# Optimization experiments

Hardware: AMD Instinct MI355X
Metric: run time of the kernel (lower is better)

## Reference

```python
import jax, jax.numpy as jnp
import numpy as np
from jax import lax

# Model config (matches init_kwargs)
SEL = [128, 128]          # radial neighbors per type
A_SEL = [16, 16]          # angular neighbors per type
LAYERS = [256, 256, 256]  # hidden layer sizes, final output dim is 1
N_ATOMS = 4096
N_TYPES = 2
D_DESC = sum(SEL) + 3 * sum(A_SEL)  # 352
BOX = 40.0
EPS = 1e-16


def setup_inputs() -> dict:
    key = jax.random.key(0)
    ks = jax.random.split(key, 16)
    xyz = jax.random.uniform(ks[0], (N_ATOMS, 3), jnp.float32) * BOX
    box_size = jnp.full((3,), BOX, jnp.float32)
    atomtypes = jax.random.randint(ks[1], (N_ATOMS,), 0, N_TYPES, jnp.int32)
    dims = [D_DESC] + LAYERS + [1]
    params = {}
    ki = 2
    for l in range(len(dims) - 1):
        params[f'w{l+1}'] = (jax.random.normal(ks[ki], (N_TYPES, dims[l], dims[l+1]), jnp.float32)
                             / np.sqrt(dims[l]).astype(np.float32))
        params[f'b{l+1}'] = jnp.zeros((N_TYPES, dims[l+1]), jnp.float32)
        ki += 1
    return {'xyz': xyz, 'box_size': box_size, 'atomtypes': atomtypes, **params}


def _descriptors(xyz, box_size, atomtypes):
    """PBC distance matrix + per-type top-k neighbors + DeePMD local-frame descriptor."""
    N = xyz.shape[0]
    # minimum-image displacement (N, N, 3) and distance (N, N)
    dm = xyz[:, None, :] - xyz[None, :, :] + EPS
    dm = dm - box_size * jnp.round(dm / box_size)
    dist = jnp.sqrt(jnp.sum(dm * dm, axis=-1))
    diag = jnp.eye(N, dtype=bool)

    blocks, a_xyz_l, a_dist_l = [], [], []
    lf_dist = lf_idx = None
    for j, selj in enumerate(SEL):
        mask = (atomtypes == j)[None, :] & (~diag)
        dists = jnp.where(mask, dist, jnp.inf)
        # full torch.sort only ever uses the first max(selj, a_selj, 2) columns -> top_k
        k = max(selj, A_SEL[j], 2)
        neg_top, idx = lax.top_k(-dists, k)
        sd = -neg_top  # sorted ascending distances, (N, k)
        if j == 0:
            lf_dist, lf_idx = sd[:, :2], idx[:, :2]
        else:
            cd = jnp.concatenate([lf_dist, sd[:, :2]], axis=1)
            ci = jnp.concatenate([lf_idx, idx[:, :2]], axis=1)
            order = jnp.argsort(cd, axis=1)
            lf_dist = jnp.take_along_axis(cd, order, axis=1)[:, :2]
            lf_idx = jnp.take_along_axis(ci, order, axis=1)[:, :2]
        blocks.append(1.0 / (sd[:, :selj] + EPS))  # inverse-distance radial block
        a_xyz_l.append(jnp.take_along_axis(dm, idx[:, :A_SEL[j], None], axis=1))
        a_dist_l.append(sd[:, :A_SEL[j]])

    a_xyz = jnp.concatenate(a_xyz_l, axis=1)    # (N, sum(a_sel), 3)
    a_dist = jnp.concatenate(a_dist_l, axis=1)  # (N, sum(a_sel))

    # local frame from the two globally nearest neighbors
    l_xyz = jnp.take_along_axis(dm, lf_idx[:, :, None], axis=1) / (lf_dist[:, :, None] + EPS)
    a_n = a_xyz / (a_dist[:, :, None] + EPS)
    r0, r1 = l_xyz[:, 0, :], l_xyz[:, 1, :]
    dot = jnp.sum(r0 * r1, axis=-1, keepdims=True)
    v2 = r1 - dot * r0
    v2 = v2 / jnp.linalg.norm(v2, axis=-1, keepdims=True)
    v3 = jnp.cross(r0, r1)
    v3 = v3 / jnp.linalg.norm(v3, axis=-1, keepdims=True)
    A = jnp.stack([r0, v2, v3], axis=-2)  # (N, 3, 3) rotation to local frame
    rot = jnp.einsum('nij,nkj->nki', A, a_n) / (a_dist[:, :, None] + EPS)  # second 1/r as in source
    return jnp.concatenate(blocks + [rot.reshape(N, 3 * sum(A_SEL))], axis=1)


def reference(xyz, box_size, atomtypes, w1, b1, w2, b2, w3, b3, w4, b4):
    # self.norm is zeros-mean / ones-std -> normalization is the identity
    desc = _descriptors(xyz, box_size, atomtypes)  # (N, D_DESC)
    # evaluate both type-specific MLPs on all atoms, then select per atom type
    h = jnp.tanh(jnp.einsum('nd,tdh->tnh', desc, w1) + b1[:, None, :])
    h = jnp.tanh(jnp.einsum('tnh,thg->tng', h, w2) + b2[:, None, :])
    h = jnp.tanh(jnp.einsum('tng,tgf->tnf', h, w3) + b3[:, None, :])
    out = jnp.einsum('tnf,tfo->tno', h, w4) + b4[:, None, :]  # (T, N, 1)
    energies = out[atomtypes, jnp.arange(desc.shape[0]), 0]
    return jnp.sum(energies)
```

## Files before the change

### kernel.cpp

```cpp
#include <hip/hip_runtime.h>
#include <hip/hip_bf16.h>

#define N_ATOMS 4096
#define NSLAB 32
#define PSTRIDE 8192
#define KSTEPS_TOTAL 27
typedef unsigned long long ull;
typedef __attribute__((ext_vector_type(8))) __bf16 bf16x8;
typedef __attribute__((ext_vector_type(4))) float f32x4;
typedef __attribute__((ext_vector_type(8))) unsigned short u16x8;

__device__ __forceinline__ float wrapr(float d, float box, float rbox) {
    return d - box * rintf(d * rbox);
}

__device__ __forceinline__ float ftanh(float x) {
    float t = __expf(2.0f * x);
    return 1.0f - 2.0f * __builtin_amdgcn_rcpf(t + 1.0f);
}

__global__ __launch_bounds__(256) void fill_kernel(
    const float* __restrict__ xyz, const int* __restrict__ types,
    int* __restrict__ slabOffG, int* __restrict__ cntG,
    int* __restrict__ lists, int* __restrict__ posArr,
    float4* __restrict__ packed, float* __restrict__ out,
    const float* __restrict__ w1, const float* __restrict__ w2,
    const float* __restrict__ w3, __hip_bfloat16* __restrict__ Wp)
{
    const int bid = blockIdx.x;
    const int tid = threadIdx.x;

    if (bid < 16) {
        __shared__ int lhAll[64];
        __shared__ int lhPre[64];
        __shared__ int base[64];
        __shared__ int cur[64];
        __shared__ int cntS[2];

        if (tid < 64) { lhAll[tid] = 0; lhPre[tid] = 0; cur[tid] = 0; }
        __syncthreads();

        const int myBase = bid * 256;
        for (int m = tid; m < N_ATOMS; m += 256) {
            int t = types[m];
            int slab = min(NSLAB - 1, (int)(xyz[3*m+2] * (NSLAB / 40.0f)));
            int ts = t * NSLAB + slab;
            atomicAdd(&lhAll[ts], 1);
            if (m < myBase) atomicAdd(&lhPre[ts], 1);
        }
        __syncthreads();

        if (tid < 64) {
            int tot = lhAll[tid];
            int v = tot;
            #pragma unroll
            for (int off = 1; off < 32; off <<= 1) {
                int u = __shfl_up(v, off);
                if ((tid & 31) >= off) v += u;
            }
            base[tid] = v - tot;
            int t = tid >> 5, s = tid & 31;
            if (s == 31) cntS[t] = v;
            if (bid == 0) {
                slabOffG[t * (NSLAB + 1) + s + 1] = v;
                if (s == 0)  slabOffG[t * (NSLAB + 1)] = 0;
                if (s == 31) cntG[t] = v;
            }
        }
        if (bid == 0 && tid == 0) out[0] = 0.0f;
        __syncthreads();

        int i = myBase + tid;
        int t = types[i];
        float z = xyz[3*i+2];
        int slab = min(NSLAB - 1, (int)(z * (NSLAB / 40.0f)));
        int ts = t * NSLAB + slab;
        int idx = base[ts] + lhPre[ts] + atomicAdd(&cur[ts], 1);
        lists[t * N_ATOMS + idx] = i;
        posArr[i] = idx;
        float4 pv = make_float4(xyz[3*i+0], xyz[3*i+1], z,
                                __uint_as_float((unsigned)i));
        packed[t * PSTRIDE + idx] = pv;
        packed[t * PSTRIDE + idx + cntS[t]] = pv;
    } else {
        int idx = (bid - 16) * 256 + tid;
        int n = idx & 255;
        int k = (idx >> 8) % 864;
        int t = idx / (864 * 256);
        int ksg, kr; float v;
        if (k < 352)      { kr = k;       ksg = kr >> 5;        v = w1[((size_t)t*352 + kr)*256 + n]; }
        else if (k < 608) { kr = k - 352; ksg = 11 + (kr >> 5); v = w2[((size_t)t*256 + kr)*256 + n]; }
        else              { kr = k - 608; ksg = 19 + (kr >> 5); v = w3[((size_t)t*256 + kr)*256 + n]; }
        int l  = (((kr & 31) >> 3) << 4) | (n & 15);
        int e  = kr & 7;
        int nt = n >> 4;
        size_t dst = ((((size_t)t*KSTEPS_TOTAL + ksg)*16 + nt) << 9) + (l << 3) + e;
        Wp[dst] = __float2bfloat16(v);
    }
}

__global__ __launch_bounds__(256) void select_kernel(
    const float* __restrict__ xyz, const float* __restrict__ box,
    const int* __restrict__ cnt, const float4* __restrict__ packed,
    const int* __restrict__ slabOffG,
    const int* __restrict__ types, const int* __restrict__ posArr,
    __hip_bfloat16* __restrict__ descB, float* __restrict__ aX,
    float* __restrict__ aD, float* __restrict__ lfD, int* __restrict__ lfJ)
{
    __shared__ ull sortedk[512];
    __shared__ int hist[256];
    __shared__ int basev[256];
    __shared__ int wsum[4];

    const int i   = blockIdx.x >> 1;
    const int t   = blockIdx.x & 1;
    const int tid = threadIdx.x;
    const int n   = cnt[t];
    const float bx = box[0], by = box[1], bz = box[2];
    const float rbx = 1.0f/bx, rby = 1.0f/by, rbz = 1.0f/bz;
    const float xi = xyz[3*i+0], yi = xyz[3*i+1], zi = xyz[3*i+2];
    const unsigned ibits = (unsigned)i;
    const float4* pk = packed + t * PSTRIDE;
    const int* soff = slabOffG + t * (NSLAB + 1);

    float T = __powf(38.2f * bx * by * bz / (float)n, 0.6666667f);
    float Twin = -1.0f, scale = 1.0f;
    int A = 0, L = n;
    int count = 0;
    float d2r[10];

    for (int attempt = 0; attempt < 8; ++attempt) {
        if (T > Twin) {
            float r = sqrtf(T);
            int slo = (int)floorf((zi - r) * (NSLAB / 40.0f)) - 1;
            int shi = (int)floorf((zi + r) * (NSLAB / 40.0f)) + 1;
            int nsl = shi - slo + 1;
            if (nsl >= NSLAB) { A = 0; L = n; }
            else {
                int ss = slo & (NSLAB - 1);
                A = soff[ss];
                int send = ss + nsl;
                L = (send <= NSLAB) ? (soff[send] - A)
                                    : (n - A) + soff[send - NSLAB];
            }
            Twin = T;
            scale = 256.0f / Twin;
            #pragma unroll
            for (int c = 0; c < 10; ++c) {
                d2r[c] = __builtin_inff();
                if ((c << 8) < L) {
                    int m = tid + (c << 8);
                    if (m < L) {
                        float4 p = pk[A + m];
                        if (__float_as_uint(p.w) != ibits) {
                            float ax_ = fabsf(xi - p.x);
                            float ay_ = fabsf(yi - p.y);
                            float az_ = fabsf(zi - p.z);
                            float mx = fminf(ax_, bx - ax_);
                            float my = fminf(ay_, by - ay_);
                            float mz = fminf(az_, bz - az_);
                            d2r[c] = mx*mx + my*my + mz*mz;
                        }
                    }
                }
            }
        }

        hist[tid] = 0;
        __syncthreads();
        #pragma unroll
        for (int c = 0; c < 10; ++c) {
            if (d2r[c] < T)
                atomicAdd(&hist[min(255, (int)(d2r[c] * scale))], 1);
        }
        __syncthreads();
        int h = hist[tid];
        int v = h;
        #pragma unroll
        for (int off = 1; off < 64; off <<= 1) {
            int u = __shfl_up(v, off);
            if ((tid & 63) >= off) v += u;
        }
        if ((tid & 63) == 63) wsum[tid >> 6] = v;
        __syncthreads();
        int woff = 0;
        #pragma unroll
        for (int w2 = 0; w2 < 3; ++w2) if (w2 < (tid >> 6)) woff += wsum[w2];
        basev[tid] = v + woff - h;
        count = wsum[0] + wsum[1] + wsum[2] + wsum[3];
        __syncthreads();
        if (count >= 128 && count <= 511) break;
        T *= (count < 128) ? 1.9f : 0.6f;
    }

    #pragma unroll
    for (int c = 0; c < 10; ++c) {
        if (d2r[c] < T) {
            int b = min(255, (int)(d2r[c] * scale));
            int pp = atomicAdd(&basev[b], 1);
            if (pp < 512) {
                int m = tid + (c << 8);
                unsigned j = __float_as_uint(pk[A + m].w);
                sortedk[pp] = ((ull)__float_as_uint(d2r[c]) << 12) | j;
            }
        }
    }
    __syncthreads();
    const int cnt2 = min(count, 512);

    const int ti = types[i];
    const int pi = posArr[i];
    __hip_bfloat16* drow = descB + ((size_t)ti * N_ATOMS + pi) * 256;
    for (int s = tid; s < cnt2; s += 256) {
        ull k = sortedk[s];
        float d2 = __uint_as_float((unsigned)(k >> 12));
        int b = min(255, (int)(d2 * scale));
        int hh = hist[b];
        int r = s;
        if (hh > 1) {
            int bs = basev[b] - hh;
            int hi2 = min(bs + hh, cnt2);
            r = bs;
            for (int x = bs; x < hi2; ++x) r += (sortedk[x] < k) ? 1 : 0;
        }
        if (r < 128) {
            int j = (int)(k & 0xFFF);
            float dist = sqrtf(d2);
            drow[t * 128 + r] = __float2bfloat16(1.0f / (dist + 1e-16f));
            if (r < 16) {
                float dx = wrapr(xi - xyz[3*j+0], bx, rbx);
                float dy = wrapr(yi - xyz[3*j+1], by, rby);
                float dz = wrapr(zi - xyz[3*j+2], bz, rbz);
                int s2 = i * 32 + t * 16 + r;
                aX[3*s2+0] = dx; aX[3*s2+1] = dy; aX[3*s2+2] = dz;
                aD[s2] = dist;
            }
            if (r < 2) {
                lfD[i * 4 + t * 2 + r] = dist;
                lfJ[i * 4 + t * 2 + r] = j;
            }
        }
    }
}

__global__ __launch_bounds__(256) void mlp_fused_kernel(
    const int* __restrict__ cnt, const int* __restrict__ lists,
    const float* __restrict__ xyz, const float* __restrict__ box,
    const float* __restrict__ aX, const float* __restrict__ aD,
    const float* __restrict__ lfD, const int* __restrict__ lfJ,
    const __hip_bfloat16* __restrict__ descB,
    const __hip_bfloat16* __restrict__ Wp,
    const float* __restrict__ b1, const float* __restrict__ b2,
    const float* __restrict__ b3,
    const float* __restrict__ w4, const float* __restrict__ b4,
    float* __restrict__ out)
{
    __shared__ __hip_bfloat16 Dld[16 * 360];
    __shared__ __hip_bfloat16 Hld[16 * 264];
    __shared__ float b1s[256], b2s[256], b3s[256], w4s[256];
    __shared__ float red[4][16];
    __shared__ float Am[8][12];
    __shared__ int atoms[8];

    const int t   = blockIdx.y;
    const int n_t = cnt[t];
    const int p0  = blockIdx.x * 8;
    if (p0 >= n_t) return;
    const int nv  = min(8, n_t - p0);
    const int tid = threadIdx.x;
    const int w   = tid >> 6;
    const int l   = tid & 63;
    const int lane15 = l & 15;
    const float bx = box[0], by = box[1], bz = box[2];
    const float rbx = 1.0f/bx, rby = 1.0f/by, rbz = 1.0f/bz;

    b1s[tid] = b1[t * 256 + tid];
    b2s[tid] = b2[t * 256 + tid];
    b3s[tid] = b3[t * 256 + tid];
    w4s[tid] = w4[t * 256 + tid];
    if (tid < 8)
        atoms[tid] = (tid < nv) ? lists[t * N_ATOMS + p0 + tid] : -1;

    for (int c = tid; c < 16 * 44; c += 256) {
        int row = c / 44, kc = c - row * 44;
        u16x8 v = {0,0,0,0,0,0,0,0};
        if (row < nv && kc < 32)
            v = *(const u16x8*)&descB[((size_t)t*N_ATOMS + p0 + row)*256 + kc*8];
        *(u16x8*)&Dld[row * 360 + kc * 8] = v;
    }
    __syncthreads();

    if (tid < 8 && atoms[tid] >= 0) {
        const int a = atoms[tid];
        const float xi = xyz[3*a+0], yi = xyz[3*a+1], zi = xyz[3*a+2];
        float cd[4]; int cj[4];
        #pragma unroll
        for (int c = 0; c < 4; ++c) { cd[c] = lfD[a*4+c]; cj[c] = lfJ[a*4+c]; }
        int i0 = 0; float bm = cd[0];
        for (int c = 1; c < 4; ++c) if (cd[c] < bm) { bm = cd[c]; i0 = c; }
        int i1 = -1; float b1v = 3.4e38f;
        for (int c = 0; c < 4; ++c) { if (c == i0) continue; if (cd[c] < b1v) { b1v = cd[c]; i1 = c; } }

        int ja = cj[i0], jb = cj[i1];
        float da = cd[i0], db = cd[i1];
        float r0x = wrapr(xi - xyz[3*ja+0], bx, rbx) / (da + 1e-16f);
        float r0y = wrapr(yi - xyz[3*ja+1], by, rby) / (da + 1e-16f);
        float r0z = wrapr(zi - xyz[3*ja+2], bz, rbz) / (da + 1e-16f);
        float r1x = wrapr(xi - xyz[3*jb+0], bx, rbx) / (db + 1e-16f);
        float r1y = wrapr(yi - xyz[3*jb+1], by, rby) / (db + 1e-16f);
        float r1z = wrapr(zi - xyz[3*jb+2], bz, rbz) / (db + 1e-16f);
        float dot = r0x*r1x + r0y*r1y + r0z*r1z;
        float v2x = r1x - dot*r0x, v2y = r1y - dot*r0y, v2z = r1z - dot*r0z;
        float n2 = sqrtf(v2x*v2x + v2y*v2y + v2z*v2z);
        v2x /= n2; v2y /= n2; v2z /= n2;
        float v3x = r0y*r1z - r0z*r1y;
        float v3y = r0z*r1x - r0x*r1z;
        float v3z = r0x*r1y - r0y*r1x;
        float n3 = sqrtf(v3x*v3x + v3y*v3y + v3z*v3z);
        v3x /= n3; v3y /= n3; v3z /= n3;
        Am[tid][0]=r0x; Am[tid][1]=r0y; Am[tid][2]=r0z;
        Am[tid][3]=v2x; Am[tid][4]=v2y; Am[tid][5]=v2z;
        Am[tid][6]=v3x; Am[tid][7]=v3y; Am[tid][8]=v3z;
    }
    __syncthreads();

    if (tid < 128) {
        const int q = tid >> 4, s = tid & 15;
        const int a = atoms[q];
        if (a >= 0) {
            #pragma unroll
            for (int half = 0; half < 2; ++half) {
                int ss = s + (half << 4);
                int sidx = a * 32 + ss;
                float d  = aD[sidx];
                float dn = d + 1e-16f;
                float ax = aX[3*sidx+0] / dn;
                float ay = aX[3*sidx+1] / dn;
                float az = aX[3*sidx+2] / dn;
                float o0 = (Am[q][0]*ax + Am[q][1]*ay + Am[q][2]*az) / dn;
                float o1 = (Am[q][3]*ax + Am[q][4]*ay + Am[q][5]*az) / dn;
                float o2 = (Am[q][6]*ax + Am[q][7]*ay + Am[q][8]*az) / dn;
                Dld[q*360 + 256 + 3*ss + 0] = __float2bfloat16(o0);
                Dld[q*360 + 256 + 3*ss + 1] = __float2bfloat16(o1);
                Dld[q*360 + 256 + 3*ss + 2] = __float2bfloat16(o2);
            }
        }
    }
    __syncthreads();

    const __hip_bfloat16* wpt = Wp + (((size_t)t * KSTEPS_TOTAL * 16 + (w << 2)) << 9);
    const int aoff = ((l >> 4) << 3);
    const int rb   = ((l >> 4) << 2);

    f32x4 acc0 = {0,0,0,0}, acc1 = {0,0,0,0}, acc2 = {0,0,0,0}, acc3 = {0,0,0,0};

#define KSTEP(SRC, STRIDE, KSG) { \
    bf16x8 a = *(const bf16x8*)&SRC[lane15 * STRIDE + (ks << 5) + aoff]; \
    const __hip_bfloat16* wk = wpt + (((size_t)(KSG) << 13)) + (l << 3); \
    bf16x8 bv0 = *(const bf16x8*)(wk); \
    bf16x8 bv1 = *(const bf16x8*)(wk + 512); \
    bf16x8 bv2 = *(const bf16x8*)(wk + 1024); \
    bf16x8 bv3 = *(const bf16x8*)(wk + 1536); \
    acc0 = __builtin_amdgcn_mfma_f32_16x16x32_bf16(a, bv0, acc0, 0, 0, 0); \
    acc1 = __builtin_amdgcn_mfma_f32_16x16x32_bf16(a, bv1, acc1, 0, 0, 0); \
    acc2 = __builtin_amdgcn_mfma_f32_16x16x32_bf16(a, bv2, acc2, 0, 0, 0); \
    acc3 = __builtin_amdgcn_mfma_f32_16x16x32_bf16(a, bv3, acc3, 0, 0, 0); }

#define STORE_H(ACC, NT, DST, STRIDE, BS) if (rb < nv) { \
    int n = (w << 6) + ((NT) << 4) + lane15; \
    float bb = BS[n]; \
    DST[(rb + 0) * STRIDE + n] = __float2bfloat16(ftanh(ACC[0] + bb)); \
    DST[(rb + 1) * STRIDE + n] = __float2bfloat16(ftanh(ACC[1] + bb)); \
    DST[(rb + 2) * STRIDE + n] = __float2bfloat16(ftanh(ACC[2] + bb)); \
    DST[(rb + 3) * STRIDE + n] = __float2bfloat16(ftanh(ACC[3] + bb)); }

    #pragma unroll 2
    for (int ks = 0; ks < 11; ++ks) KSTEP(Dld, 360, ks)
    STORE_H(acc0, 0, Hld, 264, b1s)
    STORE_H(acc1, 1, Hld, 264, b1s)
    STORE_H(acc2, 2, Hld, 264, b1s)
    STORE_H(acc3, 3, Hld, 264, b1s)
    __syncthreads();

    acc0 = (f32x4){0,0,0,0}; acc1 = acc0; acc2 = acc0; acc3 = acc0;
    #pragma unroll 2
    for (int ks = 0; ks < 8; ++ks) KSTEP(Hld, 264, 11 + ks)
    __syncthreads();
    STORE_H(acc0, 0, Dld, 360, b2s)
    STORE_H(acc1, 1, Dld, 360, b2s)
    STORE_H(acc2, 2, Dld, 360, b2s)
    STORE_H(acc3, 3, Dld, 360, b2s)
    __syncthreads();

    acc0 = (f32x4){0,0,0,0}; acc1 = acc0; acc2 = acc0; acc3 = acc0;
    #pragma unroll 2
    for (int ks = 0; ks < 8; ++ks) KSTEP(Dld, 360, 19 + ks)

    float s0 = 0.f, s1 = 0.f, s2 = 0.f, s3 = 0.f;
#define EPART(ACC, NT) if (rb < nv) { \
    int n = (w << 6) + ((NT) << 4) + lane15; \
    float wv = w4s[n]; float bb = b3s[n]; \
    s0 += ftanh(ACC[0] + bb) * wv; s1 += ftanh(ACC[1] + bb) * wv; \
    s2 += ftanh(ACC[2] + bb) * wv; s3 += ftanh(ACC[3] + bb) * wv; }
    EPART(acc0, 0) EPART(acc1, 1) EPART(acc2, 2) EPART(acc3, 3)

    #pragma unroll
    for (int off = 1; off <= 8; off <<= 1) {
        s0 += __shfl_xor(s0, off);
        s1 += __shfl_xor(s1, off);
        s2 += __shfl_xor(s2, off);
        s3 += __shfl_xor(s3, off);
    }
    if (lane15 == 0) {
        red[w][rb + 0] = s0;
        red[w][rb + 1] = s1;
        red[w][rb + 2] = s2;
        red[w][rb + 3] = s3;
    }
    __syncthreads();

    if (tid < 16) {
        float e = red[0][tid] + red[1][tid] + red[2][tid] + red[3][tid];
        e = (tid < nv) ? (e + b4[t]) : 0.0f;
        #pragma unroll
        for (int off = 1; off <= 8; off <<= 1) e += __shfl_xor(e, off);
        if (tid == 0) atomicAdd(out, e);
    }
#undef KSTEP
#undef STORE_H
#undef EPART
}

extern "C" void kernel_launch(void* const* d_in, const int* in_sizes, int n_in,
                              void* d_out, int out_size, void* d_ws, size_t ws_size,
                              hipStream_t stream) {
    const float* xyz   = (const float*)d_in[0];
    const float* box   = (const float*)d_in[1];
    const int*   types = (const int*)  d_in[2];
    const float* w1 = (const float*)d_in[3];
    const float* b1 = (const float*)d_in[4];
    const float* w2 = (const float*)d_in[5];
    const float* b2 = (const float*)d_in[6];
    const float* w3 = (const float*)d_in[7];
    const float* b3 = (const float*)d_in[8];
    const float* w4 = (const float*)d_in[9];
    const float* b4 = (const float*)d_in[10];
    float* out = (float*)d_out;

    float* p = (float*)d_ws;
    int*    cnt      = (int*)p;        p += 16;
    int*    slabOffG = (int*)p;        p += 68;
    int*    posArr   = (int*)p;        p += N_ATOMS;
    int*    lists    = (int*)p;        p += 2 * N_ATOMS;
    p += 12;
    float4* packed   = (float4*)p;     p += 2 * PSTRIDE * 4;
    float*  lfD      = p;              p += 4 * N_ATOMS;
    int*    lfJ      = (int*)p;        p += 4 * N_ATOMS;
    float*  aX       = p;              p += 96 * N_ATOMS;
    float*  aD       = p;              p += 32 * N_ATOMS;
    __hip_bfloat16* descB = (__hip_bfloat16*)p;
    p += (size_t)2 * N_ATOMS * 256 / 2;
    __hip_bfloat16* Wp = (__hip_bfloat16*)p;
    p += (size_t)2 * KSTEPS_TOTAL * 16 * 512 / 2;

    fill_kernel<<<16 + (2 * 864 * 256) / 256, 256, 0, stream>>>(
        xyz, types, slabOffG, cnt, lists, posArr, packed, out, w1, w2, w3, Wp);
    select_kernel<<<2 * N_ATOMS, 256, 0, stream>>>(
        xyz, box, cnt, packed, slabOffG, types, posArr, descB, aX, aD, lfD, lfJ);
    dim3 g(N_ATOMS / 8, 2);
    mlp_fused_kernel<<<g, 256, 0, stream>>>(cnt, lists, xyz, box, aX, aD, lfD, lfJ,
                                            descB, Wp, b1, b2, b3, w4, b4, out);
}
```

Before: 67.66 us.

## Map one wavefront per atom-type selection task instead of one block

The neighbor-selection kernel now gives each 64-lane wavefront its own (atom, type) task, with per-wave shared histograms and sort buffers. This removes all block-level __syncthreads and cross-wave scans and launches a quarter as many blocks. The histogram shrinks from 256 to 64 bins, so ties within a bin get longer intra-bin rank loops. Each lane now caches 24 distances in registers and recomputes any beyond 1536 candidates, which raises register pressure and adds redundant distance work for large windows.

```diff
diff --git a/kernel.cpp b/kernel.cpp
--- a/kernel.cpp
+++ b/kernel.cpp
@@ -107,15 +107,22 @@
     __hip_bfloat16* __restrict__ descB, float* __restrict__ aX,
     float* __restrict__ aD, float* __restrict__ lfD, int* __restrict__ lfJ)
 {
-    __shared__ ull sortedk[512];
-    __shared__ int hist[256];
-    __shared__ int basev[256];
-    __shared__ int wsum[4];
-
-    const int i   = blockIdx.x >> 1;
-    const int t   = blockIdx.x & 1;
+    __shared__ ull skAll[4][512];
+    __shared__ int histAll[4][64];
+    __shared__ int baseAll[4][64];
+
     const int tid = threadIdx.x;
+    const int wv  = tid >> 6;
+    const int ln  = tid & 63;
+    const int task = blockIdx.x * 4 + wv;
+    const int i   = task >> 1;
+    const int t   = task & 1;
     const int n   = cnt[t];
+
+    ull* sk    = skAll[wv];
+    int* hist  = histAll[wv];
+    int* basev = baseAll[wv];
+
     const float bx = box[0], by = box[1], bz = box[2];
     const float rbx = 1.0f/bx, rby = 1.0f/by, rbz = 1.0f/bz;
     const float xi = xyz[3*i+0], yi = xyz[3*i+1], zi = xyz[3*i+2];
@@ -127,7 +134,19 @@
     float Twin = -1.0f, scale = 1.0f;
     int A = 0, L = n;
     int count = 0;
-    float d2r[10];
+    float d2r[24];
+
+#define DIST(mm, dst) { \
+    float4 p = pk[A + (mm)]; \
+    dst = __builtin_inff(); \
+    if (__float_as_uint(p.w) != ibits) { \
+        float ax_ = fabsf(xi - p.x); \
+        float ay_ = fabsf(yi - p.y); \
+        float az_ = fabsf(zi - p.z); \
+        float mx = fminf(ax_, bx - ax_); \
+        float my = fminf(ay_, by - ay_); \
+        float mz = fminf(az_, bz - az_); \
+        dst = mx*mx + my*my + mz*mz; } }
 
     for (int attempt = 0; attempt < 8; ++attempt) {
         if (T > Twin) {
@@ -144,84 +163,79 @@
                                     : (n - A) + soff[send - NSLAB];
             }
             Twin = T;
-            scale = 256.0f / Twin;
             #pragma unroll
-            for (int c = 0; c < 10; ++c) {
-                d2r[c] = __builtin_inff();
-                if ((c << 8) < L) {
-                    int m = tid + (c << 8);
-                    if (m < L) {
-                        float4 p = pk[A + m];
-                        if (__float_as_uint(p.w) != ibits) {
-                            float ax_ = fabsf(xi - p.x);
-                            float ay_ = fabsf(yi - p.y);
-                            float az_ = fabsf(zi - p.z);
-                            float mx = fminf(ax_, bx - ax_);
-                            float my = fminf(ay_, by - ay_);
-                            float mz = fminf(az_, bz - az_);
-                            d2r[c] = mx*mx + my*my + mz*mz;
-                        }
-                    }
+            for (int s = 0; s < 24; ++s) {
+                d2r[s] = __builtin_inff();
+                if ((s << 6) < L) {
+                    int m = ln + (s << 6);
+                    if (m < L) DIST(m, d2r[s])
                 }
             }
         }
-
-        hist[tid] = 0;
-        __syncthreads();
+        scale = 64.0f / T;
+
+        hist[ln] = 0;
         #pragma unroll
-        for (int c = 0; c < 10; ++c) {
-            if (d2r[c] < T)
-                atomicAdd(&hist[min(255, (int)(d2r[c] * scale))], 1);
-        }
-        __syncthreads();
-        int h = hist[tid];
+        for (int s = 0; s < 24; ++s) {
+            if (d2r[s] < T)
+                atomicAdd(&hist[min(63, (int)(d2r[s] * scale))], 1);
+        }
+        for (int m = 1536 + ln; m < L; m += 64) {
+            float d2; DIST(m, d2)
+            if (d2 < T) atomicAdd(&hist[min(63, (int)(d2 * scale))], 1);
+        }
+        int h = hist[ln];
         int v = h;
         #pragma unroll
         for (int off = 1; off < 64; off <<= 1) {
             int u = __shfl_up(v, off);
-            if ((tid & 63) >= off) v += u;
-        }
-        if ((tid & 63) == 63) wsum[tid >> 6] = v;
-        __syncthreads();
-        int woff = 0;
-        #pragma unroll
-        for (int w2 = 0; w2 < 3; ++w2) if (w2 < (tid >> 6)) woff += wsum[w2];
-        basev[tid] = v + woff - h;
-        count = wsum[0] + wsum[1] + wsum[2] + wsum[3];
-        __syncthreads();
+            if (ln >= off) v += u;
+        }
+        count = __shfl(v, 63);
+        basev[ln] = v - h;
         if (count >= 128 && count <= 511) break;
         T *= (count < 128) ? 1.9f : 0.6f;
     }
 
     #pragma unroll
-    for (int c = 0; c < 10; ++c) {
-        if (d2r[c] < T) {
-            int b = min(255, (int)(d2r[c] * scale));
+    for (int s = 0; s < 24; ++s) {
+        if (d2r[s] < T) {
+            int b = min(63, (int)(d2r[s] * scale));
             int pp = atomicAdd(&basev[b], 1);
             if (pp < 512) {
-                int m = tid + (c << 8);
+                int m = ln + (s << 6);
                 unsigned j = __float_as_uint(pk[A + m].w);
-                sortedk[pp] = ((ull)__float_as_uint(d2r[c]) << 12) | j;
-            }
-        }
-    }
-    __syncthreads();
+                sk[pp] = ((ull)__float_as_uint(d2r[s]) << 12) | j;
+            }
+        }
+    }
+    for (int m = 1536 + ln; m < L; m += 64) {
+        float d2; DIST(m, d2)
+        if (d2 < T) {
+            int b = min(63, (int)(d2 * scale));
+            int pp = atomicAdd(&basev[b], 1);
+            if (pp < 512) {
+                unsigned j = __float_as_uint(pk[A + m].w);
+                sk[pp] = ((ull)__float_as_uint(d2) << 12) | j;
+            }
+        }
+    }
     const int cnt2 = min(count, 512);
 
     const int ti = types[i];
     const int pi = posArr[i];
     __hip_bfloat16* drow = descB + ((size_t)ti * N_ATOMS + pi) * 256;
-    for (int s = tid; s < cnt2; s += 256) {
-        ull k = sortedk[s];
+    for (int s2 = ln; s2 < cnt2; s2 += 64) {
+        ull k = sk[s2];
         float d2 = __uint_as_float((unsigned)(k >> 12));
-        int b = min(255, (int)(d2 * scale));
+        int b = min(63, (int)(d2 * scale));
         int hh = hist[b];
-        int r = s;
+        int r = s2;
         if (hh > 1) {
             int bs = basev[b] - hh;
             int hi2 = min(bs + hh, cnt2);
             r = bs;
-            for (int x = bs; x < hi2; ++x) r += (sortedk[x] < k) ? 1 : 0;
+            for (int x = bs; x < hi2; ++x) r += (sk[x] < k) ? 1 : 0;
         }
         if (r < 128) {
             int j = (int)(k & 0xFFF);
@@ -231,9 +245,9 @@
                 float dx = wrapr(xi - xyz[3*j+0], bx, rbx);
                 float dy = wrapr(yi - xyz[3*j+1], by, rby);
                 float dz = wrapr(zi - xyz[3*j+2], bz, rbz);
-                int s2 = i * 32 + t * 16 + r;
-                aX[3*s2+0] = dx; aX[3*s2+1] = dy; aX[3*s2+2] = dz;
-                aD[s2] = dist;
+                int s3 = i * 32 + t * 16 + r;
+                aX[3*s3+0] = dx; aX[3*s3+1] = dy; aX[3*s3+2] = dz;
+                aD[s3] = dist;
             }
             if (r < 2) {
                 lfD[i * 4 + t * 2 + r] = dist;
@@ -241,6 +255,7 @@
             }
         }
     }
+#undef DIST
 }
 
 __global__ __launch_bounds__(256) void mlp_fused_kernel(
@@ -465,7 +480,7 @@
 
     fill_kernel<<<16 + (2 * 864 * 256) / 256, 256, 0, stream>>>(
         xyz, types, slabOffG, cnt, lists, posArr, packed, out, w1, w2, w3, Wp);
-    select_kernel<<<2 * N_ATOMS, 256, 0, stream>>>(
+    select_kernel<<<2 * N_ATOMS / 4, 256, 0, stream>>>(
         xyz, box, cnt, packed, slabOffG, types, posArr, descB, aX, aD, lfD, lfJ);
     dim3 g(N_ATOMS / 8, 2);
     mlp_fused_kernel<<<g, 256, 0, stream>>>(cnt, lists, xyz, box, aX, aD, lfD, lfJ,
```

Measured after the change: 82.60 us. +22.1%, slower.
